# Kernel optimization log

Hardware: AMD Instinct MI355X
Metric: run time of the kernel (lower is better)

The kernel has to match this reference:

```python
import jax, jax.numpy as jnp
import numpy as np

D_MODEL = 2048
N_HEADS = 16
N_KV = 4
HEAD_DIM = D_MODEL // N_HEADS  # 128
KV_DIM = N_KV * HEAD_DIM       # 512
CLIP = 8.0
EPS = 1e-5
THETA = 500000.0


def setup_inputs() -> dict:
    key = jax.random.key(0)
    ks = jax.random.split(key, 12)
    B, T = 2, 2048
    std = 0.02
    return {
        "x": jax.random.normal(ks[0], (B, T, D_MODEL), jnp.float32),
        "wq": jax.random.normal(ks[1], (D_MODEL, D_MODEL), jnp.float32) * std,
        "bq": jnp.zeros((D_MODEL,), jnp.float32),
        "wk": jax.random.normal(ks[2], (KV_DIM, D_MODEL), jnp.float32) * std,
        "bk": jnp.zeros((KV_DIM,), jnp.float32),
        "wv": jax.random.normal(ks[3], (KV_DIM, D_MODEL), jnp.float32) * std,
        "bv": jnp.zeros((KV_DIM,), jnp.float32),
        "wo": jax.random.normal(ks[4], (D_MODEL, D_MODEL), jnp.float32) * std,
        "bo": jnp.zeros((D_MODEL,), jnp.float32),
        "q_gamma": jnp.ones((D_MODEL,), jnp.float32),
        "q_beta": jnp.zeros((D_MODEL,), jnp.float32),
        "k_gamma": jnp.ones((KV_DIM,), jnp.float32),
        "k_beta": jnp.zeros((KV_DIM,), jnp.float32),
    }


def _layernorm(x, gamma, beta):
    mu = jnp.mean(x, axis=-1, keepdims=True)
    var = jnp.mean(jnp.square(x - mu), axis=-1, keepdims=True)
    return (x - mu) * jax.lax.rsqrt(var + EPS) * gamma + beta


def _rope(q, k):
    # q: (B,T,H,Dh), k: (B,T,Hkv,Dh); non-interleaved rotate-half RoPE
    T = q.shape[1]
    half = HEAD_DIM // 2
    inv_freq = 1.0 / (THETA ** (jnp.arange(0, half, dtype=jnp.float32) * 2.0 / HEAD_DIM))
    freqs = jnp.arange(T, dtype=jnp.float32)[:, None] * inv_freq[None, :]  # (T, half)
    emb = jnp.concatenate([freqs, freqs], axis=-1)  # (T, Dh)
    cos = jnp.cos(emb)[None, :, None, :]
    sin = jnp.sin(emb)[None, :, None, :]

    def rot_half(x):
        x1, x2 = x[..., :half], x[..., half:]
        return jnp.concatenate([-x2, x1], axis=-1)

    q = q * cos + rot_half(q) * sin
    k = k * cos + rot_half(k) * sin
    return q, k


def reference(x, wq, bq, wk, bk, wv, bv, wo, bo, q_gamma, q_beta, k_gamma, k_beta):
    B, T, _ = x.shape
    q = x @ wq.T + bq            # (B,T,D)
    k = x @ wk.T + bk            # (B,T,KV_DIM)
    v = x @ wv.T + bv
    q = jnp.clip(q, -CLIP, CLIP)
    k = jnp.clip(k, -CLIP, CLIP)
    v = jnp.clip(v, -CLIP, CLIP)
    q = _layernorm(q, q_gamma, q_beta)
    k = _layernorm(k, k_gamma, k_beta)
    q = q.reshape(B, T, N_HEADS, HEAD_DIM)
    k = k.reshape(B, T, N_KV, HEAD_DIM)
    v = v.reshape(B, T, N_KV, HEAD_DIM)
    q, k = _rope(q, k)
    # to (B,H,T,Dh)
    q = q.transpose(0, 2, 1, 3)
    k = k.transpose(0, 2, 1, 3)
    v = v.transpose(0, 2, 1, 3)
    g = N_HEADS // N_KV
    # GQA repeat_interleave via broadcast: (B,Hkv,T,Dh) -> (B,H,T,Dh)
    k = jnp.broadcast_to(k[:, :, None], (B, N_KV, g, T, HEAD_DIM)).reshape(B, N_HEADS, T, HEAD_DIM)
    v = jnp.broadcast_to(v[:, :, None], (B, N_KV, g, T, HEAD_DIM)).reshape(B, N_HEADS, T, HEAD_DIM)
    scale = 1.0 / jnp.sqrt(jnp.float32(HEAD_DIM))
    scores = jnp.einsum('bhqd,bhkd->bhqk', q, k) * scale
    causal = jnp.tril(jnp.ones((T, T), dtype=bool))
    scores = jnp.where(causal[None, None], scores, jnp.finfo(scores.dtype).min)
    att = jax.nn.softmax(scores, axis=-1)
    out = jnp.einsum('bhqk,bhkd->bhqd', att, v)     # (B,H,T,Dh)
    out = out.transpose(0, 2, 1, 3).reshape(B, T, D_MODEL)
    return out @ wo.T + bo
```

## Files before the change

kernel.cpp:

```cpp
#include <hip/hip_runtime.h>
#include <hip/hip_bf16.h>
#include <math.h>

typedef __bf16 bf16;
typedef __attribute__((ext_vector_type(8))) bf16 bf16x8;
typedef __attribute__((ext_vector_type(4))) bf16 bf16x4;
typedef __attribute__((ext_vector_type(2))) bf16 bf16x2;
typedef __attribute__((ext_vector_type(4))) float f32x4;

#define LOG2E 1.4426950408889634f
#define LOG2_THETA 18.931568569324174f

#if __has_builtin(__builtin_amdgcn_exp2f)
#define EXP2F __builtin_amdgcn_exp2f
#else
#define EXP2F exp2f
#endif

__device__ inline void async_cp16(const void* gptr, void* lptr) {
  __builtin_amdgcn_global_load_lds(
      (const __attribute__((address_space(1))) unsigned int*)gptr,
      (__attribute__((address_space(3))) unsigned int*)lptr, 16, 0, 0);
}

__global__ __launch_bounds__(256) void cast_all(
    const float* __restrict__ x,  const float* __restrict__ wq,
    const float* __restrict__ wk, const float* __restrict__ wv,
    const float* __restrict__ wo, bf16* __restrict__ xb,
    bf16* __restrict__ wqkvb, bf16* __restrict__ wob) {
  const int bx = blockIdx.x;
  const size_t gi = ((size_t)bx * 256 + threadIdx.x) * 8;
  const float* src;
  bf16* dst;
  if (bx < 4096)      { src = x  + gi;              dst = xb + gi; }
  else if (bx < 6144) { src = wq + (gi -  8388608); dst = wqkvb + (gi - 8388608); }
  else if (bx < 6656) { src = wk + (gi - 12582912); dst = wqkvb + 4194304 + (gi - 12582912); }
  else if (bx < 7168) { src = wv + (gi - 13631488); dst = wqkvb + 5242880 + (gi - 13631488); }
  else                { src = wo + (gi - 14680064); dst = wob + (gi - 14680064); }
  float4 a = *(const float4*)(src);
  float4 b = *(const float4*)(src + 4);
  bf16x8 o;
  o[0] = (bf16)a.x; o[1] = (bf16)a.y; o[2] = (bf16)a.z; o[3] = (bf16)a.w;
  o[4] = (bf16)b.x; o[5] = (bf16)b.y; o[6] = (bf16)b.z; o[7] = (bf16)b.w;
  *(bf16x8*)dst = o;
}

template <typename OUT_T, bool QKV, bool CLIP>
__global__ __launch_bounds__(256) void gemm_bt(
    const bf16* __restrict__ A, const bf16* __restrict__ W,
    const float* __restrict__ b0, const float* __restrict__ b1,
    const float* __restrict__ b2, OUT_T* __restrict__ C,
    int M, int N, int K) {
  __shared__ bf16 As[128 * 64];
  __shared__ bf16 Bs[128 * 64];
  const int m0 = blockIdx.x * 128, n0 = blockIdx.y * 128;
  const int t = threadIdx.x;
  const int w = t >> 6, lane = t & 63, quad = lane >> 4, l15 = lane & 15;
  const int sw = l15 & 7;
  const int wm = (w >> 1) * 64, wn = (w & 1) * 64;

  f32x4 acc[4][4];
#pragma unroll
  for (int i = 0; i < 4; i++)
#pragma unroll
    for (int j = 0; j < 4; j++) acc[i][j] = (f32x4)0.0f;

  int soff[4];
#pragma unroll
  for (int i = 0; i < 4; i++) {
    const int c = w * 256 + i * 64 + lane;
    const int r = c >> 3;
    const int sl = (c & 7) ^ (r & 7);
    soff[i] = r * K + sl * 8;
  }
  const bf16* Abase = A + (size_t)m0 * K;
  const bf16* Wbase = W + (size_t)n0 * K;

  for (int k0 = 0; k0 < K; k0 += 64) {
#pragma unroll
    for (int i = 0; i < 4; i++) {
      const int dst = (w * 256 + i * 64) * 16;
      async_cp16(Abase + k0 + soff[i], (char*)As + dst);
      async_cp16(Wbase + k0 + soff[i], (char*)Bs + dst);
    }
    __syncthreads();

#pragma unroll
    for (int kk = 0; kk < 2; kk++) {
      bf16x8 af[4], bfr[4];
#pragma unroll
      for (int i = 0; i < 4; i++)
        af[i] = *(const bf16x8*)(As + (wm + i * 16 + l15) * 64 +
                                 (((kk * 4 + quad) ^ sw) * 8));
#pragma unroll
      for (int j = 0; j < 4; j++)
        bfr[j] = *(const bf16x8*)(Bs + (wn + j * 16 + l15) * 64 +
                                  (((kk * 4 + quad) ^ sw) * 8));
#pragma unroll
      for (int i = 0; i < 4; i++)
#pragma unroll
        for (int j = 0; j < 4; j++)
          acc[i][j] = __builtin_amdgcn_mfma_f32_16x16x32_bf16(af[i], bfr[j], acc[i][j], 0, 0, 0);
    }
    __syncthreads();
  }

#pragma unroll
  for (int i = 0; i < 4; i++)
#pragma unroll
    for (int j = 0; j < 4; j++) {
      const int col = n0 + wn + j * 16 + l15;
      float bval;
      if (QKV) {
        if (col < 2048) bval = b0[col];
        else if (col < 2560) bval = b1[col - 2048];
        else bval = b2[col - 2560];
      } else {
        bval = b0[col];
      }
#pragma unroll
      for (int r = 0; r < 4; r++) {
        const int row = m0 + wm + i * 16 + quad * 4 + r;
        float v = acc[i][j][r] + bval;
        if (CLIP) v = fminf(fmaxf(v, -8.0f), 8.0f);
        C[(size_t)row * N + col] = (OUT_T)v;
      }
    }
}

__global__ __launch_bounds__(256) void fused_mid(
    const bf16* __restrict__ X, const float* __restrict__ qg,
    const float* __restrict__ qb, const float* __restrict__ kg,
    const float* __restrict__ kb, bf16* __restrict__ Qr,
    bf16* __restrict__ Kr, bf16* __restrict__ Vt) {
  __shared__ float smf[2056];
  __shared__ bf16 smt[64][136];
  const int bx = blockIdx.x;
  const int tid = threadIdx.x;
  const int w = tid >> 6, lane = tid & 63;
  float* red = smf + 2048;

  if (bx < 4096) {
    const int row = bx, b = row >> 11, tpos = row & 2047;
    const bf16* x = X + (size_t)row * 3072;
    bf16x8 xi = *(const bf16x8*)(x + tid * 8);
    float v[8];
    float s = 0.0f;
#pragma unroll
    for (int e = 0; e < 8; e++) { v[e] = (float)xi[e]; s += v[e]; }
#pragma unroll
    for (int m = 32; m >= 1; m >>= 1) s += __shfl_xor(s, m, 64);
    if (lane == 0) red[w] = s;
    __syncthreads();
    const float mean = (red[0] + red[1] + red[2] + red[3]) * (1.0f / 2048.0f);
    float vs = 0.0f;
#pragma unroll
    for (int e = 0; e < 8; e++) { float d = v[e] - mean; vs += d * d; }
#pragma unroll
    for (int m = 32; m >= 1; m >>= 1) vs += __shfl_xor(vs, m, 64);
    if (lane == 0) red[4 + w] = vs;
    __syncthreads();
    const float var = (red[4] + red[5] + red[6] + red[7]) * (1.0f / 2048.0f);
    const float rstd = rsqrtf(var + 1e-5f);
#pragma unroll
    for (int e = 0; e < 8; e++) {
      const int c = tid * 8 + e;
      const float y = (v[e] - mean) * rstd * qg[c] + qb[c];
      smf[c] = y; v[e] = y;
    }
    __syncthreads();
    const int c0 = tid * 8;
    const int h = c0 >> 7;
    bf16x8 ov;
#pragma unroll
    for (int e = 0; e < 8; e++) {
      const int c = c0 + e, d = c & 127, i = d & 63;
      const float inv = exp2f((float)i * (-LOG2_THETA / 64.0f));
      float sn, cs;
      sincosf((float)tpos * inv, &sn, &cs);
      const float rot = (d < 64) ? -smf[c + 64] : smf[c - 64];
      ov[e] = (bf16)(v[e] * cs + rot * sn);
    }
    *(bf16x8*)(Qr + ((size_t)(b * 16 + h) * 2048 + tpos) * 128 + (c0 & 127)) = ov;
  } else if (bx < 8192) {
    const int row = bx - 4096, b = row >> 11, tpos = row & 2047;
    const bf16* x = X + (size_t)row * 3072 + 2048;
    bf16x2 xi = *(const bf16x2*)(x + tid * 2);
    float v0 = (float)xi[0], v1 = (float)xi[1];
    float s = v0 + v1;
#pragma unroll
    for (int m = 32; m >= 1; m >>= 1) s += __shfl_xor(s, m, 64);
    if (lane == 0) red[w] = s;
    __syncthreads();
    const float mean = (red[0] + red[1] + red[2] + red[3]) * (1.0f / 512.0f);
    float d0 = v0 - mean, d1 = v1 - mean;
    float vs = d0 * d0 + d1 * d1;
#pragma unroll
    for (int m = 32; m >= 1; m >>= 1) vs += __shfl_xor(vs, m, 64);
    if (lane == 0) red[4 + w] = vs;
    __syncthreads();
    const float var = (red[4] + red[5] + red[6] + red[7]) * (1.0f / 512.0f);
    const float rstd = rsqrtf(var + 1e-5f);
    const int c0 = tid * 2;
    float y0 = d0 * rstd * kg[c0] + kb[c0];
    float y1 = d1 * rstd * kg[c0 + 1] + kb[c0 + 1];
    smf[c0] = y0; smf[c0 + 1] = y1;
    __syncthreads();
    const int kv = c0 >> 7;
    float yy[2] = {y0, y1};
    bf16x2 ov;
#pragma unroll
    for (int e = 0; e < 2; e++) {
      const int c = c0 + e, d = c & 127, i = d & 63;
      const float inv = exp2f((float)i * (-LOG2_THETA / 64.0f));
      float sn, cs;
      sincosf((float)tpos * inv, &sn, &cs);
      const float rot = (d < 64) ? -smf[c + 64] : smf[c - 64];
      ov[e] = (bf16)(yy[e] * cs + rot * sn);
    }
    *(bf16x2*)(Kr + ((size_t)(b * 4 + kv) * 2048 + tpos) * 128 + (c0 & 127)) = ov;
  } else {
    const int idx = bx - 8192;
    const int b = idx >> 7, kv = (idx >> 5) & 3, t0 = (idx & 31) * 64;
#pragma unroll
    for (int i = 0; i < 4; i++) {
      const int c = i * 256 + tid;
      const int r = c >> 4, d8 = (c & 15) * 8;
      *(bf16x8*)&smt[r][d8] =
          *(const bf16x8*)(X + (size_t)(b * 2048 + t0 + r) * 3072 + 2560 + kv * 128 + d8);
    }
    __syncthreads();
#pragma unroll
    for (int i = 0; i < 4; i++) {
      const int c = i * 256 + tid;
      const int d = c >> 3, t8 = (c & 7) * 8;
      bf16x8 o;
#pragma unroll
      for (int j = 0; j < 8; j++) o[j] = smt[t8 + j][d];
      *(bf16x8*)(Vt + (size_t)((b * 4 + kv) * 128 + d) * 2048 + t0 + t8) = o;
    }
  }
}

__global__ __launch_bounds__(512) void flash_attn(
    const bf16* __restrict__ Q, const bf16* __restrict__ Kt,
    const bf16* __restrict__ Vt, bf16* __restrict__ O) {
  __shared__ bf16 Ks[2][64][128];
  __shared__ bf16 Vs[2][128][64];

  const int p = blockIdx.x;
  const int hp = blockIdx.y;
  const int b = blockIdx.z;
  const int kv = hp >> 1;
  const int tid = threadIdx.x;
  const int w = tid >> 6, lane = tid & 63, quad = lane >> 4, l15 = lane & 15;
  const int strip = w & 3, hl = w >> 2;
  const int h = hp * 2 + hl;

  const bf16* Kb = Kt + (size_t)(b * 4 + kv) * 2048 * 128;
  const bf16* Vb = Vt + (size_t)(b * 4 + kv) * 128 * 2048;

  int koff[2], voff[2];
#pragma unroll
  for (int i = 0; i < 2; i++) {
    const int c = w * 128 + i * 64 + lane;
    const int kr = c >> 4, kp = c & 15;
    koff[i] = kr * 128 + ((kp ^ (kr & 15)) * 8);
    const int vd = c >> 3, vp = c & 7;
    voff[i] = vd * 2048 + ((vp ^ (vd & 7)) * 8);
  }

  const float cexp = 0.08838834764831845f * LOG2E;
  bf16x8 onesA;
#pragma unroll
  for (int i = 0; i < 8; i++) onesA[i] = (bf16)1.0f;

  const int srcA = l15 + ((quad & 1) << 5);
  const int srcB = srcA + 16;
  const bool hiSel = (quad >> 1) != 0;

#pragma unroll 1
  for (int pass = 0; pass < 2; pass++) {
    const int qb = (pass == 0) ? (31 - p) : p;
    const int q0 = qb * 64;
    const int nkt = qb + 1;
    const int qrow = q0 + strip * 16 + l15;

    const bf16* Qb = Q + ((size_t)(b * 16 + h) * 2048 + qrow) * 128;
    bf16x8 aq[4];
#pragma unroll
    for (int kk = 0; kk < 4; kk++) aq[kk] = *(const bf16x8*)(Qb + kk * 32 + quad * 8);

    f32x4 o[8];
#pragma unroll
    for (int dt = 0; dt < 8; dt++) o[dt] = (f32x4)0.0f;
    f32x4 o8 = (f32x4)0.0f;

    __syncthreads();
#pragma unroll
    for (int i = 0; i < 2; i++) {
      const int dst = (w * 128 + i * 64) * 16;
      async_cp16(Kb + koff[i], (char*)Ks + dst);
      async_cp16(Vb + voff[i], (char*)Vs + dst);
    }

#pragma unroll 1
    for (int kt = 0; kt < nkt; kt++) {
      const int k0 = kt * 64;
      const int cur = kt & 1;
      __syncthreads();

      if (kt + 1 < nkt) {
        const size_t kn = (size_t)(k0 + 64);
#pragma unroll
        for (int i = 0; i < 2; i++) {
          const int dst = (w * 128 + i * 64) * 16;
          async_cp16(Kb + kn * 128 + koff[i], (char*)Ks + (cur ^ 1) * 16384 + dst);
          async_cp16(Vb + kn + voff[i], (char*)Vs + (cur ^ 1) * 16384 + dst);
        }
      }

      const bf16* Kcur = &Ks[cur][0][0];
      const bf16* Vcur = &Vs[cur][0][0];

      f32x4 s4t[4];
#pragma unroll
      for (int j = 0; j < 4; j++) {
        f32x4 acc = (f32x4)0.0f;
        const int krow = j * 16 + l15;
#pragma unroll
        for (int kk = 0; kk < 4; kk++) {
          bf16x8 bk = *(const bf16x8*)(Kcur + krow * 128 + (((kk * 4 + quad) ^ l15) * 8));
          acc = __builtin_amdgcn_mfma_f32_16x16x32_bf16(bk, aq[kk], acc, 0, 0, 0);
        }
        s4t[j] = acc;
      }

      const bool diag = (kt == qb);
      unsigned pp[4][2];
#pragma unroll
      for (int j = 0; j < 4; j++) {
        const int kbase = k0 + j * 16 + quad * 4;
        float pv[4];
#pragma unroll
        for (int r = 0; r < 4; r++) {
          float e = EXP2F(s4t[j][r] * cexp);
          if (diag && (kbase + r > qrow)) e = 0.0f;
          pv[r] = e;
        }
        union { bf16x2 h; unsigned u; } u0, u1;
        u0.h[0] = (bf16)pv[0]; u0.h[1] = (bf16)pv[1];
        u1.h[0] = (bf16)pv[2]; u1.h[1] = (bf16)pv[3];
        pp[j][0] = u0.u; pp[j][1] = u1.u;
      }

#pragma unroll
      for (int kk = 0; kk < 2; kk++) {
        const int ja = 2 * kk, jb = 2 * kk + 1;
        unsigned a00 = (unsigned)__shfl((int)pp[ja][0], srcA, 64);
        unsigned a01 = (unsigned)__shfl((int)pp[ja][1], srcA, 64);
        unsigned a10 = (unsigned)__shfl((int)pp[jb][0], srcA, 64);
        unsigned a11 = (unsigned)__shfl((int)pp[jb][1], srcA, 64);
        unsigned b00 = (unsigned)__shfl((int)pp[ja][0], srcB, 64);
        unsigned b01 = (unsigned)__shfl((int)pp[ja][1], srcB, 64);
        unsigned b10 = (unsigned)__shfl((int)pp[jb][0], srcB, 64);
        unsigned b11 = (unsigned)__shfl((int)pp[jb][1], srcB, 64);
        union { unsigned u[4]; bf16x8 v; } ub;
        ub.u[0] = hiSel ? a10 : a00;
        ub.u[1] = hiSel ? a11 : a01;
        ub.u[2] = hiSel ? b10 : b00;
        ub.u[3] = hiSel ? b11 : b01;
#pragma unroll
        for (int dt = 0; dt < 8; dt++) {
          const int d = dt * 16 + l15;
          bf16x8 av = *(const bf16x8*)(Vcur + d * 64 + (((kk * 4 + quad) ^ (d & 7)) * 8));
          o[dt] = __builtin_amdgcn_mfma_f32_16x16x32_bf16(av, ub.v, o[dt], 0, 0, 0);
        }
        o8 = __builtin_amdgcn_mfma_f32_16x16x32_bf16(onesA, ub.v, o8, 0, 0, 0);
      }
    }

    const float rinv = 1.0f / o8[0];
    bf16* Ob = O + ((size_t)(b * 2048) + qrow) * 2048 + h * 128;
#pragma unroll
    for (int dt = 0; dt < 8; dt++) {
      bf16x4 pk;
#pragma unroll
      for (int r = 0; r < 4; r++) pk[r] = (bf16)(o[dt][r] * rinv);
      *(bf16x4*)(Ob + dt * 16 + quad * 4) = pk;
    }
  }
}

extern "C" void kernel_launch(void* const* d_in, const int* in_sizes, int n_in,
                              void* d_out, int out_size, void* d_ws, size_t ws_size,
                              hipStream_t stream) {
  const float* x   = (const float*)d_in[0];
  const float* wq  = (const float*)d_in[1];
  const float* bq  = (const float*)d_in[2];
  const float* wk  = (const float*)d_in[3];
  const float* bk  = (const float*)d_in[4];
  const float* wv  = (const float*)d_in[5];
  const float* bv  = (const float*)d_in[6];
  const float* wo  = (const float*)d_in[7];
  const float* bo  = (const float*)d_in[8];
  const float* qg  = (const float*)d_in[9];
  const float* qbt = (const float*)d_in[10];
  const float* kg  = (const float*)d_in[11];
  const float* kbt = (const float*)d_in[12];
  float* out = (float*)d_out;

  char* ws = (char*)d_ws;
  if (ws_size < (size_t)88080384) return;
  bf16* xb    = (bf16*)(ws);
  bf16* wqkvb = (bf16*)(ws + 16777216);
  bf16* wob   = (bf16*)(ws + 29360128);
  bf16* qkvb  = (bf16*)(ws + 37748736);
  bf16* Qr    = (bf16*)(ws + 62914560);
  bf16* Kr    = (bf16*)(ws + 79691776);
  bf16* Vt    = (bf16*)(ws + 83886080);
  bf16* At    = (bf16*)(ws);

  cast_all<<<9216, 256, 0, stream>>>(x, wq, wk, wv, wo, xb, wqkvb, wob);
  gemm_bt<bf16, true, true><<<dim3(32, 24), 256, 0, stream>>>(
      xb, wqkvb, bq, bk, bv, qkvb, 4096, 3072, 2048);
  fused_mid<<<8448, 256, 0, stream>>>(qkvb, qg, qbt, kg, kbt, Qr, Kr, Vt);
  flash_attn<<<dim3(16, 8, 2), 512, 0, stream>>>(Qr, Kr, Vt, At);
  gemm_bt<float, false, false><<<dim3(32, 16), 256, 0, stream>>>(
      At, wob, bo, nullptr, nullptr, out, 4096, 2048, 2048);
}
```

Measured before the change: 330.9 us.

## Restructure flash attention to one head per 256-thread block with 32-key tiles

Each flash-attention block now handles a single head with 4 waves instead of two heads with 8 waves, and the key/value tiles shrink from 64 to 32 keys. The V shared-memory swizzle is rewritten for the narrower tile, and the causal diagonal check now covers the last two tiles. This halves shared memory per block and doubles the block count, aiming for higher occupancy and less waste on diagonal tiles. In exchange there are twice as many loop iterations and barriers per query block, and K/V tiles are no longer shared across two heads, so global and LDS traffic rises.

```diff
diff --git a/kernel.cpp b/kernel.cpp
--- a/kernel.cpp
+++ b/kernel.cpp
@@ -242,20 +242,17 @@
   }
 }
 
-__global__ __launch_bounds__(512) void flash_attn(
+__global__ __launch_bounds__(256) void flash_attn(
     const bf16* __restrict__ Q, const bf16* __restrict__ Kt,
     const bf16* __restrict__ Vt, bf16* __restrict__ O) {
-  __shared__ bf16 Ks[2][64][128];
-  __shared__ bf16 Vs[2][128][64];
+  __shared__ bf16 Ks[2][32][128];
+  __shared__ bf16 Vs[2][128][32];
 
   const int p = blockIdx.x;
-  const int hp = blockIdx.y;
-  const int b = blockIdx.z;
-  const int kv = hp >> 1;
+  const int h = blockIdx.y, b = blockIdx.z;
+  const int kv = h >> 2;
   const int tid = threadIdx.x;
   const int w = tid >> 6, lane = tid & 63, quad = lane >> 4, l15 = lane & 15;
-  const int strip = w & 3, hl = w >> 2;
-  const int h = hp * 2 + hl;
 
   const bf16* Kb = Kt + (size_t)(b * 4 + kv) * 2048 * 128;
   const bf16* Vb = Vt + (size_t)(b * 4 + kv) * 128 * 2048;
@@ -266,8 +263,8 @@
     const int c = w * 128 + i * 64 + lane;
     const int kr = c >> 4, kp = c & 15;
     koff[i] = kr * 128 + ((kp ^ (kr & 15)) * 8);
-    const int vd = c >> 3, vp = c & 7;
-    voff[i] = vd * 2048 + ((vp ^ (vd & 7)) * 8);
+    const int vd = c >> 2, vp = c & 3;
+    voff[i] = vd * 2048 + ((vp ^ ((vd ^ (vd >> 2)) & 3)) * 8);
   }
 
   const float cexp = 0.08838834764831845f * LOG2E;
@@ -283,8 +280,8 @@
   for (int pass = 0; pass < 2; pass++) {
     const int qb = (pass == 0) ? (31 - p) : p;
     const int q0 = qb * 64;
-    const int nkt = qb + 1;
-    const int qrow = q0 + strip * 16 + l15;
+    const int nkt = 2 * (qb + 1);
+    const int qrow = q0 + w * 16 + l15;
 
     const bf16* Qb = Q + ((size_t)(b * 16 + h) * 2048 + qrow) * 128;
     bf16x8 aq[4];
@@ -306,26 +303,26 @@
 
 #pragma unroll 1
     for (int kt = 0; kt < nkt; kt++) {
-      const int k0 = kt * 64;
+      const int k0 = kt * 32;
       const int cur = kt & 1;
       __syncthreads();
 
       if (kt + 1 < nkt) {
-        const size_t kn = (size_t)(k0 + 64);
+        const size_t kn = (size_t)(k0 + 32);
 #pragma unroll
         for (int i = 0; i < 2; i++) {
           const int dst = (w * 128 + i * 64) * 16;
-          async_cp16(Kb + kn * 128 + koff[i], (char*)Ks + (cur ^ 1) * 16384 + dst);
-          async_cp16(Vb + kn + voff[i], (char*)Vs + (cur ^ 1) * 16384 + dst);
+          async_cp16(Kb + kn * 128 + koff[i], (char*)Ks + (cur ^ 1) * 8192 + dst);
+          async_cp16(Vb + kn + voff[i], (char*)Vs + (cur ^ 1) * 8192 + dst);
         }
       }
 
       const bf16* Kcur = &Ks[cur][0][0];
       const bf16* Vcur = &Vs[cur][0][0];
 
-      f32x4 s4t[4];
-#pragma unroll
-      for (int j = 0; j < 4; j++) {
+      f32x4 s4t[2];
+#pragma unroll
+      for (int j = 0; j < 2; j++) {
         f32x4 acc = (f32x4)0.0f;
         const int krow = j * 16 + l15;
 #pragma unroll
@@ -336,10 +333,10 @@
         s4t[j] = acc;
       }
 
-      const bool diag = (kt == qb);
-      unsigned pp[4][2];
-#pragma unroll
-      for (int j = 0; j < 4; j++) {
+      const bool diag = (kt >= nkt - 2);
+      unsigned pp[2][2];
+#pragma unroll
+      for (int j = 0; j < 2; j++) {
         const int kbase = k0 + j * 16 + quad * 4;
         float pv[4];
 #pragma unroll
@@ -348,23 +345,21 @@
           if (diag && (kbase + r > qrow)) e = 0.0f;
           pv[r] = e;
         }
-        union { bf16x2 h; unsigned u; } u0, u1;
-        u0.h[0] = (bf16)pv[0]; u0.h[1] = (bf16)pv[1];
-        u1.h[0] = (bf16)pv[2]; u1.h[1] = (bf16)pv[3];
+        union { bf16x2 hh; unsigned u; } u0, u1;
+        u0.hh[0] = (bf16)pv[0]; u0.hh[1] = (bf16)pv[1];
+        u1.hh[0] = (bf16)pv[2]; u1.hh[1] = (bf16)pv[3];
         pp[j][0] = u0.u; pp[j][1] = u1.u;
       }
 
-#pragma unroll
-      for (int kk = 0; kk < 2; kk++) {
-        const int ja = 2 * kk, jb = 2 * kk + 1;
-        unsigned a00 = (unsigned)__shfl((int)pp[ja][0], srcA, 64);
-        unsigned a01 = (unsigned)__shfl((int)pp[ja][1], srcA, 64);
-        unsigned a10 = (unsigned)__shfl((int)pp[jb][0], srcA, 64);
-        unsigned a11 = (unsigned)__shfl((int)pp[jb][1], srcA, 64);
-        unsigned b00 = (unsigned)__shfl((int)pp[ja][0], srcB, 64);
-        unsigned b01 = (unsigned)__shfl((int)pp[ja][1], srcB, 64);
-        unsigned b10 = (unsigned)__shfl((int)pp[jb][0], srcB, 64);
-        unsigned b11 = (unsigned)__shfl((int)pp[jb][1], srcB, 64);
+      {
+        unsigned a00 = (unsigned)__shfl((int)pp[0][0], srcA, 64);
+        unsigned a01 = (unsigned)__shfl((int)pp[0][1], srcA, 64);
+        unsigned a10 = (unsigned)__shfl((int)pp[1][0], srcA, 64);
+        unsigned a11 = (unsigned)__shfl((int)pp[1][1], srcA, 64);
+        unsigned b00 = (unsigned)__shfl((int)pp[0][0], srcB, 64);
+        unsigned b01 = (unsigned)__shfl((int)pp[0][1], srcB, 64);
+        unsigned b10 = (unsigned)__shfl((int)pp[1][0], srcB, 64);
+        unsigned b11 = (unsigned)__shfl((int)pp[1][1], srcB, 64);
         union { unsigned u[4]; bf16x8 v; } ub;
         ub.u[0] = hiSel ? a10 : a00;
         ub.u[1] = hiSel ? a11 : a01;
@@ -373,7 +368,8 @@
 #pragma unroll
         for (int dt = 0; dt < 8; dt++) {
           const int d = dt * 16 + l15;
-          bf16x8 av = *(const bf16x8*)(Vcur + d * 64 + (((kk * 4 + quad) ^ (d & 7)) * 8));
+          bf16x8 av = *(const bf16x8*)(
+              Vcur + d * 32 + (((quad ^ ((d ^ (d >> 2)) & 3)) * 8)));
           o[dt] = __builtin_amdgcn_mfma_f32_16x16x32_bf16(av, ub.v, o[dt], 0, 0, 0);
         }
         o8 = __builtin_amdgcn_mfma_f32_16x16x32_bf16(onesA, ub.v, o8, 0, 0, 0);
@@ -425,7 +421,7 @@
   gemm_bt<bf16, true, true><<<dim3(32, 24), 256, 0, stream>>>(
       xb, wqkvb, bq, bk, bv, qkvb, 4096, 3072, 2048);
   fused_mid<<<8448, 256, 0, stream>>>(qkvb, qg, qbt, kg, kbt, Qr, Kr, Vt);
-  flash_attn<<<dim3(16, 8, 2), 512, 0, stream>>>(Qr, Kr, Vt, At);
+  flash_attn<<<dim3(16, 16, 2), 256, 0, stream>>>(Qr, Kr, Vt, At);
   gemm_bt<float, false, false><<<dim3(32, 16), 256, 0, stream>>>(
       At, wob, bo, nullptr, nullptr, out, 4096, 2048, 2048);
 }
```

Result: no change. 334.3 us (+1.0%).
